# Kernel optimization log

Hardware: AMD Instinct MI355X
Metric: run time of the kernel (lower is better)

Reference implementation:

```python
import jax, jax.numpy as jnp
import numpy as np

N = 50000   # nodes
E = 800000  # edges
K = 3       # hops per TAGConv


def _row_normalize(x):
    row_sum = jnp.clip(jnp.sum(x, axis=1, keepdims=True), 1e-8, None)
    return x / row_sum


def _gcn_norm(edge_index, num_nodes):
    # PyG gcn_norm with add_self_loops=False (TAGConv default), edge_weight=1
    src, dst = edge_index[0], edge_index[1]
    deg = jax.ops.segment_sum(jnp.ones((src.shape[0],), jnp.float32), dst,
                              num_segments=num_nodes)
    deg_inv_sqrt = jnp.where(deg > 0, jnp.where(deg > 0, deg, 1.0) ** -0.5, 0.0)
    return deg_inv_sqrt[src] * deg_inv_sqrt[dst]  # [E]


def _propagate(x, src, dst, norm, num_nodes):
    # out[dst] += norm * x[src]   (sparse sym-normalized SpMM)
    return jax.ops.segment_sum(norm[:, None] * x[src], dst, num_segments=num_nodes)


def _tagconv(x, edge_index, norm, W, b):
    # W: [K+1, d_in, d_out]; out = sum_k A_hat^k x @ W_k + b
    src, dst = edge_index[0], edge_index[1]
    n = x.shape[0]
    hops = [x]
    for _ in range(W.shape[0] - 1):
        hops.append(_propagate(hops[-1], src, dst, norm, n))
    H = jnp.stack(hops)  # [K+1, N, d_in]
    return jnp.einsum('knd,kdo->no', H, W) + b


def setup_inputs() -> dict:
    key = jax.random.key(0)
    k1, k2, k3, k4 = jax.random.split(key, 4)
    x = jax.random.normal(k1, (N, 128), jnp.float32)
    edge_index = jax.random.randint(k2, (2, E), 0, N, jnp.int32)
    W1 = jax.random.normal(k3, (K + 1, 128, 16), jnp.float32) * 0.1
    b1 = jnp.zeros((16,), jnp.float32)
    W2 = jax.random.normal(k4, (K + 1, 16, 64), jnp.float32) * 0.1
    b2 = jnp.zeros((64,), jnp.float32)
    return {"x": x, "edge_index": edge_index, "W1": W1, "b1": b1,
            "W2": W2, "b2": b2}


def reference(x, edge_index, W1, b1, W2, b2):
    n = x.shape[0]
    norm = _gcn_norm(edge_index, n)
    h = _row_normalize(x)
    h = jax.nn.relu(_tagconv(h, edge_index, norm, W1, b1))
    # dropout is identity in eval mode
    return _tagconv(h, edge_index, norm, W2, b2)
```

## Files before the change

kernel.cpp:

```cpp
#include <hip/hip_runtime.h>
#include <hip/hip_bf16.h>

typedef unsigned short u16;

__device__ __forceinline__ float bf2f(u16 h) {
    return __uint_as_float(((unsigned int)h) << 16);
}
__device__ __forceinline__ u16 f2bf(float f) {
    __hip_bfloat16 h = __float2bfloat16(f);
    return *reinterpret_cast<u16*>(&h);
}

#define BKT_SHIFT 7
#define BKT_SIZE  128
#define CHUNK     2048

__global__ __launch_bounds__(256) void hist_kernel(const int* __restrict__ dst,
                                                   int* __restrict__ hist,
                                                   int E, int nbA, int nbuck) {
    __shared__ int lh[512];
    for (int j = threadIdx.x; j < nbuck; j += 256) lh[j] = 0;
    __syncthreads();
    int base = blockIdx.x * CHUNK;
    int end  = min(E, base + CHUNK);
    for (int e = base + threadIdx.x; e < end; e += 256)
        atomicAdd(&lh[dst[e] >> BKT_SHIFT], 1);
    __syncthreads();
    for (int j = threadIdx.x; j < nbuck; j += 256)
        hist[j * nbA + blockIdx.x] = lh[j];
}

__global__ __launch_bounds__(256) void scanA_kernel(const int* __restrict__ in,
                                                    int* __restrict__ outp1,
                                                    int* __restrict__ bsum, int n) {
    __shared__ int lds[256];
    int i = blockIdx.x * 256 + threadIdx.x;
    int v = (i < n) ? in[i] : 0;
    lds[threadIdx.x] = v;
    __syncthreads();
    #pragma unroll
    for (int off = 1; off < 256; off <<= 1) {
        int t = (threadIdx.x >= off) ? lds[threadIdx.x - off] : 0;
        __syncthreads();
        lds[threadIdx.x] += t;
        __syncthreads();
    }
    if (i < n) outp1[i + 1] = lds[threadIdx.x];
    if (threadIdx.x == 255) bsum[blockIdx.x] = lds[255];
}
__global__ __launch_bounds__(1024) void scanB_kernel(int* __restrict__ bsum, int nb) {
    __shared__ int lds[1024];
    int t = threadIdx.x;
    int v = (t < nb) ? bsum[t] : 0;
    lds[t] = v;
    __syncthreads();
    #pragma unroll
    for (int off = 1; off < 1024; off <<= 1) {
        int u = (t >= off) ? lds[t - off] : 0;
        __syncthreads();
        lds[t] += u;
        __syncthreads();
    }
    if (t < nb) bsum[t] = lds[t] - v;
}
__global__ __launch_bounds__(256) void scanC_kernel(int* __restrict__ outp1,
                                                    const int* __restrict__ bsum, int n) {
    int i = blockIdx.x * 256 + threadIdx.x;
    if (i < n) outp1[i + 1] += bsum[blockIdx.x];
    if (i == 0) outp1[0] = 0;
}

__global__ __launch_bounds__(256) void bucket_scatter_kernel(
    const int* __restrict__ src, const int* __restrict__ dst,
    const int* __restrict__ hofs, int2* __restrict__ bucketed,
    int E, int nbA, int nbuck)
{
    __shared__ int lbase[512];
    __shared__ int lcnt[512];
    for (int j = threadIdx.x; j < nbuck; j += 256) {
        lbase[j] = hofs[j * nbA + blockIdx.x];
        lcnt[j] = 0;
    }
    __syncthreads();
    int base = blockIdx.x * CHUNK;
    int end  = min(E, base + CHUNK);
    for (int e = base + threadIdx.x; e < end; e += 256) {
        int d = dst[e];
        int b = d >> BKT_SHIFT;
        int r = atomicAdd(&lcnt[b], 1);
        bucketed[lbase[b] + r] = make_int2(src[e], d);
    }
}

__global__ __launch_bounds__(256) void csr_finalize_kernel(
    const int2* __restrict__ bucketed, const int* __restrict__ hofs,
    int* __restrict__ rowptr, float* __restrict__ dis,
    float2* __restrict__ ecolw, int E, int nbA, int nbuck, int n)
{
    __shared__ int cnt[BKT_SIZE];
    __shared__ int run[BKT_SIZE];
    __shared__ float disl[BKT_SIZE];
    int b = blockIdx.x;
    int bstart = hofs[b * nbA];
    int bend   = (b == nbuck - 1) ? E : hofs[(b + 1) * nbA];
    for (int j = threadIdx.x; j < BKT_SIZE; j += 256) cnt[j] = 0;
    __syncthreads();
    for (int i = bstart + threadIdx.x; i < bend; i += 256)
        atomicAdd(&cnt[bucketed[i].y & (BKT_SIZE - 1)], 1);
    __syncthreads();
    if (threadIdx.x == 0) {
        int runacc = 0;
        for (int j = 0; j < BKT_SIZE; ++j) {
            int c = cnt[j];
            run[j] = runacc;
            runacc += c;
        }
    }
    __syncthreads();
    for (int j = threadIdx.x; j < BKT_SIZE; j += 256) {
        int d = b * BKT_SIZE + j;
        if (d < n) {
            rowptr[d] = bstart + run[j];
            int c = cnt[j];
            float dv = (c > 0) ? rsqrtf((float)c) : 0.0f;
            dis[d] = dv;
            disl[j] = dv;
        }
    }
    if (b == 0 && threadIdx.x == 0) rowptr[n] = E;
    __syncthreads();
    for (int i = bstart + threadIdx.x; i < bend; i += 256) {
        int2 p = bucketed[i];
        int j = p.y & (BKT_SIZE - 1);
        int r = atomicAdd(&run[j], 1);
        ecolw[bstart + r] = make_float2(__int_as_float(p.x), disl[j]);
    }
}

__global__ __launch_bounds__(256) void weight_kernel(float2* __restrict__ ecolw,
                                                     const float* __restrict__ dis, int E) {
    int e = blockIdx.x * blockDim.x + threadIdx.x;
    if (e < E) {
        float2 c = ecolw[e];
        ecolw[e].y = c.y * dis[__float_as_int(c.x)];
    }
}

__global__ __launch_bounds__(256) void gemm1_bf_kernel(
    const float* __restrict__ x, const float* __restrict__ W1,
    u16* __restrict__ zb, int n, int nstride)
{
    __shared__ float As[64 * 132];
    __shared__ float Bs[64 * 64];
    __shared__ float sums[128];
    const int t  = threadIdx.x;
    const int tx = t & 15;
    const int ty = t >> 4;
    const int c  = t & 15;
    const int g  = t >> 4;
    const int block_row = blockIdx.x * 128;

    float acc[8][4];
    #pragma unroll
    for (int i = 0; i < 8; ++i)
        #pragma unroll
        for (int j = 0; j < 4; ++j) acc[i][j] = 0.f;

    for (int kp = 0; kp < 2; ++kp) {
        #pragma unroll
        for (int i = 0; i < 8; ++i) {
            int row  = g + 16 * i;
            int grow = block_row + row;
            float v0 = 0.f, v1 = 0.f, v2 = 0.f, v3 = 0.f;
            if (grow < n) {
                const float* xp = x + (long)grow * 128 + kp * 64 + c;
                v0 = xp[0]; v1 = xp[16]; v2 = xp[32]; v3 = xp[48];
            }
            As[(c +  0) * 132 + row] = v0;
            As[(c + 16) * 132 + row] = v1;
            As[(c + 32) * 132 + row] = v2;
            As[(c + 48) * 132 + row] = v3;
            float red = (v0 + v1) + (v2 + v3);
            #pragma unroll
            for (int off = 8; off > 0; off >>= 1) red += __shfl_down(red, off, 16);
            if (c == 0) { if (kp == 0) sums[row] = red; else sums[row] += red; }
        }
        #pragma unroll
        for (int i2 = 0; i2 < 4; ++i2) {
            int kk = g + 16 * i2;
            int kglob = kp * 64 + kk;
            float4 wv = *(const float4*)(W1 + (c >> 2) * 2048 + kglob * 16 + 4 * (c & 3));
            *(float4*)(Bs + kk * 64 + 4 * c) = wv;
        }
        __syncthreads();
        #pragma unroll 4
        for (int kk = 0; kk < 64; ++kk) {
            float4 a0 = *(const float4*)(As + kk * 132 + 8 * ty);
            float4 a1 = *(const float4*)(As + kk * 132 + 8 * ty + 4);
            float4 bv = *(const float4*)(Bs + kk * 64 + 4 * tx);
            float ar[8] = {a0.x, a0.y, a0.z, a0.w, a1.x, a1.y, a1.z, a1.w};
            float br[4] = {bv.x, bv.y, bv.z, bv.w};
            #pragma unroll
            for (int i = 0; i < 8; ++i)
                #pragma unroll
                for (int j = 0; j < 4; ++j)
                    acc[i][j] += ar[i] * br[j];
        }
        __syncthreads();
    }
    int plane = tx >> 2;
    int oo4   = 4 * (tx & 3);
    #pragma unroll
    for (int i = 0; i < 8; ++i) {
        int row  = 8 * ty + i;
        int grow = block_row + row;
        if (grow < n) {
            float s = 1.0f / fmaxf(sums[row], 1e-8f);
            ushort4 o;
            o.x = f2bf(acc[i][0] * s); o.y = f2bf(acc[i][1] * s);
            o.z = f2bf(acc[i][2] * s); o.w = f2bf(acc[i][3] * s);
            *(ushort4*)(zb + (long)plane * nstride + (long)grow * 16 + oo4) = o;
        }
    }
}

__global__ __launch_bounds__(256) void spmm_csr_bf_kernel(
    const u16* __restrict__ in, const u16* __restrict__ addsrc,
    u16* __restrict__ out, const int* __restrict__ rowptr,
    const float2* __restrict__ ecolw, const float* __restrict__ b,
    int relu, int n)
{
    int t = blockIdx.x * blockDim.x + threadIdx.x;
    int r = t >> 3, q = t & 7;
    if (r >= n) return;
    int e0 = rowptr[r], e1 = rowptr[r + 1];
    float ax0=0,ay0=0, ax1=0,ay1=0, ax2=0,ay2=0, ax3=0,ay3=0;
    int e = e0;
    for (; e + 4 <= e1; e += 4) {
        float2 c0 = ecolw[e], c1 = ecolw[e+1], c2 = ecolw[e+2], c3 = ecolw[e+3];
        ushort2 v0 = *((const ushort2*)(in + (size_t)__float_as_int(c0.x) * 16) + q);
        ushort2 v1 = *((const ushort2*)(in + (size_t)__float_as_int(c1.x) * 16) + q);
        ushort2 v2 = *((const ushort2*)(in + (size_t)__float_as_int(c2.x) * 16) + q);
        ushort2 v3 = *((const ushort2*)(in + (size_t)__float_as_int(c3.x) * 16) + q);
        ax0 += c0.y * bf2f(v0.x); ay0 += c0.y * bf2f(v0.y);
        ax1 += c1.y * bf2f(v1.x); ay1 += c1.y * bf2f(v1.y);
        ax2 += c2.y * bf2f(v2.x); ay2 += c2.y * bf2f(v2.y);
        ax3 += c3.y * bf2f(v3.x); ay3 += c3.y * bf2f(v3.y);
    }
    for (; e < e1; ++e) {
        float2 c0 = ecolw[e];
        ushort2 v0 = *((const ushort2*)(in + (size_t)__float_as_int(c0.x) * 16) + q);
        ax0 += c0.y * bf2f(v0.x); ay0 += c0.y * bf2f(v0.y);
    }
    float Ax = (ax0 + ax1) + (ax2 + ax3);
    float Ay = (ay0 + ay1) + (ay2 + ay3);
    if (addsrc) {
        ushort2 s = *((const ushort2*)(addsrc + (size_t)r * 16) + q);
        Ax += bf2f(s.x); Ay += bf2f(s.y);
    }
    if (b) {
        Ax += b[2 * q];
        Ay += b[2 * q + 1];
    }
    if (relu) {
        Ax = fmaxf(Ax, 0.f);
        Ay = fmaxf(Ay, 0.f);
    }
    ushort2 o; o.x = f2bf(Ax); o.y = f2bf(Ay);
    *((ushort2*)(out + (size_t)r * 16) + q) = o;
}

__global__ __launch_bounds__(256) void gemm2_bf_kernel(
    const u16* __restrict__ zb, const float* __restrict__ W2,
    const float* __restrict__ b2, float* __restrict__ out, int n, int nstride)
{
    __shared__ float As[64 * 132];
    __shared__ float Bs[64 * 64];
    const int t  = threadIdx.x;
    const int tx = t & 15;
    const int ty = t >> 4;
    const int c  = t & 15;
    const int g  = t >> 4;
    const int block_row = blockIdx.x * 128;

    float acc[8][4];
    #pragma unroll
    for (int i = 0; i < 8; ++i)
        #pragma unroll
        for (int j = 0; j < 4; ++j) acc[i][j] = 0.f;

    #pragma unroll
    for (int i = 0; i < 8; ++i) {
        int row  = g + 16 * i;
        int grow = block_row + row;
        float v0 = 0.f, v1 = 0.f, v2 = 0.f, v3 = 0.f;
        if (grow < n) {
            const u16* zp = zb + (long)grow * 16 + c;
            v0 = bf2f(zp[0]);
            v1 = bf2f(zp[(long)nstride]);
            v2 = bf2f(zp[2 * (long)nstride]);
            v3 = bf2f(zp[3 * (long)nstride]);
        }
        As[(c +  0) * 132 + row] = v0;
        As[(c + 16) * 132 + row] = v1;
        As[(c + 32) * 132 + row] = v2;
        As[(c + 48) * 132 + row] = v3;
    }
    #pragma unroll
    for (int i2 = 0; i2 < 4; ++i2) {
        int j = g + 16 * i2;
        float4 wv = *(const float4*)(W2 + j * 64 + 4 * c);
        *(float4*)(Bs + j * 64 + 4 * c) = wv;
    }
    __syncthreads();
    #pragma unroll 4
    for (int kk = 0; kk < 64; ++kk) {
        float4 a0 = *(const float4*)(As + kk * 132 + 8 * ty);
        float4 a1 = *(const float4*)(As + kk * 132 + 8 * ty + 4);
        float4 bv = *(const float4*)(Bs + kk * 64 + 4 * tx);
        float ar[8] = {a0.x, a0.y, a0.z, a0.w, a1.x, a1.y, a1.z, a1.w};
        float br[4] = {bv.x, bv.y, bv.z, bv.w};
        #pragma unroll
        for (int i = 0; i < 8; ++i)
            #pragma unroll
            for (int j = 0; j < 4; ++j)
                acc[i][j] += ar[i] * br[j];
    }
    float4 bias = *(const float4*)(b2 + 4 * tx);
    #pragma unroll
    for (int i = 0; i < 8; ++i) {
        int grow = block_row + 8 * ty + i;
        if (grow < n) {
            float4 o = make_float4(acc[i][0] + bias.x, acc[i][1] + bias.y,
                                   acc[i][2] + bias.z, acc[i][3] + bias.w);
            *(float4*)(out + (long)grow * 64 + 4 * tx) = o;
        }
    }
}

__global__ void deg_kernel(const int* __restrict__ dst, float* __restrict__ deg, int E) {
    int e = blockIdx.x * blockDim.x + threadIdx.x;
    if (e < E) atomicAdd(&deg[dst[e]], 1.0f);
}
__global__ void disf_kernel(float* __restrict__ deg, int n) {
    int i = blockIdx.x * blockDim.x + threadIdx.x;
    if (i < n) {
        float d = deg[i];
        deg[i] = (d > 0.0f) ? rsqrtf(d) : 0.0f;
    }
}
__global__ __launch_bounds__(256) void gemm1_f32_kernel(
    const float* __restrict__ x, const float* __restrict__ W1,
    float* __restrict__ z, int n, int nstride)
{
    __shared__ float As[64 * 132];
    __shared__ float Bs[64 * 64];
    __shared__ float sums[128];
    const int t  = threadIdx.x;
    const int tx = t & 15;
    const int ty = t >> 4;
    const int c  = t & 15;
    const int g  = t >> 4;
    const int block_row = blockIdx.x * 128;
    float acc[8][4];
    #pragma unroll
    for (int i = 0; i < 8; ++i)
        #pragma unroll
        for (int j = 0; j < 4; ++j) acc[i][j] = 0.f;
    for (int kp = 0; kp < 2; ++kp) {
        #pragma unroll
        for (int i = 0; i < 8; ++i) {
            int row  = g + 16 * i;
            int grow = block_row + row;
            float v0 = 0.f, v1 = 0.f, v2 = 0.f, v3 = 0.f;
            if (grow < n) {
                const float* xp = x + (long)grow * 128 + kp * 64 + c;
                v0 = xp[0]; v1 = xp[16]; v2 = xp[32]; v3 = xp[48];
            }
            As[(c +  0) * 132 + row] = v0;
            As[(c + 16) * 132 + row] = v1;
            As[(c + 32) * 132 + row] = v2;
            As[(c + 48) * 132 + row] = v3;
            float red = (v0 + v1) + (v2 + v3);
            #pragma unroll
            for (int off = 8; off > 0; off >>= 1) red += __shfl_down(red, off, 16);
            if (c == 0) { if (kp == 0) sums[row] = red; else sums[row] += red; }
        }
        #pragma unroll
        for (int i2 = 0; i2 < 4; ++i2) {
            int kk = g + 16 * i2;
            int kglob = kp * 64 + kk;
            float4 wv = *(const float4*)(W1 + (c >> 2) * 2048 + kglob * 16 + 4 * (c & 3));
            *(float4*)(Bs + kk * 64 + 4 * c) = wv;
        }
        __syncthreads();
        #pragma unroll 4
        for (int kk = 0; kk < 64; ++kk) {
            float4 a0 = *(const float4*)(As + kk * 132 + 8 * ty);
            float4 a1 = *(const float4*)(As + kk * 132 + 8 * ty + 4);
            float4 bv = *(const float4*)(Bs + kk * 64 + 4 * tx);
            float ar[8] = {a0.x, a0.y, a0.z, a0.w, a1.x, a1.y, a1.z, a1.w};
            float br[4] = {bv.x, bv.y, bv.z, bv.w};
            #pragma unroll
            for (int i = 0; i < 8; ++i)
                #pragma unroll
                for (int j = 0; j < 4; ++j)
                    acc[i][j] += ar[i] * br[j];
        }
        __syncthreads();
    }
    int plane = tx >> 2;
    int oo4   = 4 * (tx & 3);
    #pragma unroll
    for (int i = 0; i < 8; ++i) {
        int row  = 8 * ty + i;
        int grow = block_row + row;
        if (grow < n) {
            float s = 1.0f / fmaxf(sums[row], 1e-8f);
            float4 o = make_float4(acc[i][0] * s, acc[i][1] * s, acc[i][2] * s, acc[i][3] * s);
            *(float4*)(z + (long)plane * nstride + (long)grow * 16 + oo4) = o;
        }
    }
}
__global__ __launch_bounds__(256) void spmm_atomic_kernel(
    const float* __restrict__ in, float* __restrict__ out,
    const int* __restrict__ src, const int* __restrict__ dst,
    const float* __restrict__ dis, int E)
{
    int t = blockIdx.x * blockDim.x + threadIdx.x;
    int e = t >> 4, f = t & 15;
    if (e < E) {
        int s = src[e], d = dst[e];
        atomicAdd(&out[d * 16 + f], dis[s] * dis[d] * in[s * 16 + f]);
    }
}
__global__ void bias_relu_kernel(float* __restrict__ z0, const float* __restrict__ b, int total) {
    int i = blockIdx.x * blockDim.x + threadIdx.x;
    if (i < total) {
        float v = z0[i] + b[i & 15];
        z0[i] = v > 0.0f ? v : 0.0f;
    }
}
__global__ __launch_bounds__(256) void gemm2_f32_kernel(
    const float* __restrict__ z, const float* __restrict__ W2,
    const float* __restrict__ b2, float* __restrict__ out, int n, int nstride)
{
    __shared__ float As[64 * 132];
    __shared__ float Bs[64 * 64];
    const int t  = threadIdx.x;
    const int tx = t & 15;
    const int ty = t >> 4;
    const int c  = t & 15;
    const int g  = t >> 4;
    const int block_row = blockIdx.x * 128;
    float acc[8][4];
    #pragma unroll
    for (int i = 0; i < 8; ++i)
        #pragma unroll
        for (int j = 0; j < 4; ++j) acc[i][j] = 0.f;
    #pragma unroll
    for (int i = 0; i < 8; ++i) {
        int row  = g + 16 * i;
        int grow = block_row + row;
        float v0 = 0.f, v1 = 0.f, v2 = 0.f, v3 = 0.f;
        if (grow < n) {
            const float* zp = z + (long)grow * 16 + c;
            v0 = zp[0];
            v1 = zp[(long)nstride];
            v2 = zp[2 * (long)nstride];
            v3 = zp[3 * (long)nstride];
        }
        As[(c +  0) * 132 + row] = v0;
        As[(c + 16) * 132 + row] = v1;
        As[(c + 32) * 132 + row] = v2;
        As[(c + 48) * 132 + row] = v3;
    }
    #pragma unroll
    for (int i2 = 0; i2 < 4; ++i2) {
        int j = g + 16 * i2;
        float4 wv = *(const float4*)(W2 + j * 64 + 4 * c);
        *(float4*)(Bs + j * 64 + 4 * c) = wv;
    }
    __syncthreads();
    #pragma unroll 4
    for (int kk = 0; kk < 64; ++kk) {
        float4 a0 = *(const float4*)(As + kk * 132 + 8 * ty);
        float4 a1 = *(const float4*)(As + kk * 132 + 8 * ty + 4);
        float4 bv = *(const float4*)(Bs + kk * 64 + 4 * tx);
        float ar[8] = {a0.x, a0.y, a0.z, a0.w, a1.x, a1.y, a1.z, a1.w};
        float br[4] = {bv.x, bv.y, bv.z, bv.w};
        #pragma unroll
        for (int i = 0; i < 8; ++i)
            #pragma unroll
            for (int j = 0; j < 4; ++j)
                acc[i][j] += ar[i] * br[j];
    }
    float4 bias = *(const float4*)(b2 + 4 * tx);
    #pragma unroll
    for (int i = 0; i < 8; ++i) {
        int grow = block_row + 8 * ty + i;
        if (grow < n) {
            float4 o = make_float4(acc[i][0] + bias.x, acc[i][1] + bias.y,
                                   acc[i][2] + bias.z, acc[i][3] + bias.w);
            *(float4*)(out + (long)grow * 64 + 4 * tx) = o;
        }
    }
}

static inline size_t align16(size_t v) { return (v + 15) & ~(size_t)15; }

extern "C" void kernel_launch(void* const* d_in, const int* in_sizes, int n_in,
                              void* d_out, int out_size, void* d_ws, size_t ws_size,
                              hipStream_t stream) {
    const float* x   = (const float*)d_in[0];
    const int*   ei  = (const int*)d_in[1];
    const float* W1  = (const float*)d_in[2];
    const float* b1  = (const float*)d_in[3];
    const float* W2  = (const float*)d_in[4];
    const float* bb2 = (const float*)d_in[5];
    float* out = (float*)d_out;

    const int n  = in_sizes[0] / 128;
    const int E  = in_sizes[1] / 2;
    const int NS = n * 16;

    const int* srcp = ei;
    const int* dstp = ei + E;

    const int nbuck = (n + BKT_SIZE - 1) >> BKT_SHIFT;
    const int nbA   = (E + CHUNK - 1) / CHUNK;
    const int m     = nbuck * nbA;
    const int nbS   = (m + 255) / 256;

    char* wsb = (char*)d_ws;
    int*   hist   = (int*)wsb;
    int*   hofs   = (int*)(wsb + (size_t)4 * m);
    int*   bsum   = (int*)(wsb + (size_t)4 * (2 * m + 1));
    int*   rowptr = (int*)(wsb + (size_t)4 * (2 * m + 1 + 1024));
    float* dis    = (float*)(wsb + (size_t)4 * (2 * m + 1 + 1024 + n + 1));
    size_t zoffb  = align16((size_t)4 * (2 * m + 1 + 1024 + 2 * n + 1));
    u16*   zb     = (u16*)(wsb + zoffb);
    size_t bkoff  = align16(zoffb + (size_t)2 * 4 * NS);
    int2*  bucketed = (int2*)(wsb + bkoff);
    size_t ecooff = align16(bkoff + (size_t)8 * E);
    float2* ecolw = (float2*)(wsb + ecooff);
    size_t need   = ecooff + (size_t)8 * E;

    int gemm_blocks = (n + 127) / 128;

    if (ws_size >= need && nbuck <= 512 && nbS <= 1024) {
        hist_kernel<<<nbA, 256, 0, stream>>>(dstp, hist, E, nbA, nbuck);
        scanA_kernel<<<nbS, 256, 0, stream>>>(hist, hofs, bsum, m);
        scanB_kernel<<<1, 1024, 0, stream>>>(bsum, nbS);
        scanC_kernel<<<nbS, 256, 0, stream>>>(hofs, bsum, m);
        bucket_scatter_kernel<<<nbA, 256, 0, stream>>>(srcp, dstp, hofs, bucketed, E, nbA, nbuck);
        csr_finalize_kernel<<<nbuck, 256, 0, stream>>>(bucketed, hofs, rowptr, dis, ecolw, E, nbA, nbuck, n);
        weight_kernel<<<(E + 255) / 256, 256, 0, stream>>>(ecolw, dis, E);

        gemm1_bf_kernel<<<gemm_blocks, 256, 0, stream>>>(x, W1, zb, n, NS);

        int sb = (8 * n + 255) / 256;
        spmm_csr_bf_kernel<<<sb, 256, 0, stream>>>(zb + 3 * NS, zb + 2 * NS, zb + 2 * NS, rowptr, ecolw, nullptr, 0, n);
        spmm_csr_bf_kernel<<<sb, 256, 0, stream>>>(zb + 2 * NS, zb + 1 * NS, zb + 1 * NS, rowptr, ecolw, nullptr, 0, n);
        spmm_csr_bf_kernel<<<sb, 256, 0, stream>>>(zb + 1 * NS, zb,          zb,          rowptr, ecolw, b1,      1, n);
        spmm_csr_bf_kernel<<<sb, 256, 0, stream>>>(zb,          nullptr, zb + 1 * NS, rowptr, ecolw, nullptr, 0, n);
        spmm_csr_bf_kernel<<<sb, 256, 0, stream>>>(zb + 1 * NS, nullptr, zb + 2 * NS, rowptr, ecolw, nullptr, 0, n);
        spmm_csr_bf_kernel<<<sb, 256, 0, stream>>>(zb + 2 * NS, nullptr, zb + 3 * NS, rowptr, ecolw, nullptr, 0, n);

        gemm2_bf_kernel<<<gemm_blocks, 256, 0, stream>>>(zb, W2, bb2, out, n, NS);
    } else {
        float* ws = (float*)d_ws;
        float* dis2 = ws;
        size_t z2off = ((size_t)n + 3) & ~(size_t)3;
        float* z2 = ws + z2off;
        hipMemsetAsync(dis2, 0, n * sizeof(float), stream);
        deg_kernel<<<(E + 255) / 256, 256, 0, stream>>>(dstp, dis2, E);
        disf_kernel<<<(n + 255) / 256, 256, 0, stream>>>(dis2, n);
        gemm1_f32_kernel<<<gemm_blocks, 256, 0, stream>>>(x, W1, z2, n, NS);
        int sb = (16 * E + 255) / 256;
        spmm_atomic_kernel<<<sb, 256, 0, stream>>>(z2 + 3 * NS, z2 + 2 * NS, srcp, dstp, dis2, E);
        spmm_atomic_kernel<<<sb, 256, 0, stream>>>(z2 + 2 * NS, z2 + 1 * NS, srcp, dstp, dis2, E);
        spmm_atomic_kernel<<<sb, 256, 0, stream>>>(z2 + 1 * NS, z2,          srcp, dstp, dis2, E);
        bias_relu_kernel<<<(NS + 255) / 256, 256, 0, stream>>>(z2, b1, NS);
        hipMemsetAsync(z2 + NS, 0, (size_t)3 * NS * sizeof(float), stream);
        spmm_atomic_kernel<<<sb, 256, 0, stream>>>(z2,          z2 + NS,     srcp, dstp, dis2, E);
        spmm_atomic_kernel<<<sb, 256, 0, stream>>>(z2 + NS,     z2 + 2 * NS, srcp, dstp, dis2, E);
        spmm_atomic_kernel<<<sb, 256, 0, stream>>>(z2 + 2 * NS, z2 + 3 * NS, srcp, dstp, dis2, E);
        gemm2_f32_kernel<<<gemm_blocks, 256, 0, stream>>>(z2, W2, bb2, out, n, NS);
    }
}
```

Before: 215.3 us.

## Factor symmetric norm into per-node scales and drop per-edge weights

Replaces the per-edge weight array with index-only CSR columns by factoring D^-1/2 A D^-1/2 into per-node row and column scalings. Gemm1 pre-scales the propagated planes by dis, and the SpMM scales by dis (or dis squared) at the row end. The second layer writes extra pre-scaled temporaries, so the edge loop only gathers and sums. This halves edge-array traffic and removes the weight_kernel launch, at the cost of extra workspace and additional bf16 writes of the scaled copies.

```diff
diff --git a/kernel.cpp b/kernel.cpp
--- a/kernel.cpp
+++ b/kernel.cpp
@@ -2,9 +2,10 @@
 #include <hip/hip_bf16.h>
 
 typedef unsigned short u16;
+typedef unsigned int u32;
 
 __device__ __forceinline__ float bf2f(u16 h) {
-    return __uint_as_float(((unsigned int)h) << 16);
+    return __uint_as_float(((u32)h) << 16);
 }
 __device__ __forceinline__ u16 f2bf(float f) {
     __hip_bfloat16 h = __float2bfloat16(f);
@@ -95,11 +96,10 @@
 __global__ __launch_bounds__(256) void csr_finalize_kernel(
     const int2* __restrict__ bucketed, const int* __restrict__ hofs,
     int* __restrict__ rowptr, float* __restrict__ dis,
-    float2* __restrict__ ecolw, int E, int nbA, int nbuck, int n)
+    u32* __restrict__ ecol, int E, int nbA, int nbuck, int n)
 {
     __shared__ int cnt[BKT_SIZE];
     __shared__ int run[BKT_SIZE];
-    __shared__ float disl[BKT_SIZE];
     int b = blockIdx.x;
     int bstart = hofs[b * nbA];
     int bend   = (b == nbuck - 1) ? E : hofs[(b + 1) * nbA];
@@ -122,9 +122,7 @@
         if (d < n) {
             rowptr[d] = bstart + run[j];
             int c = cnt[j];
-            float dv = (c > 0) ? rsqrtf((float)c) : 0.0f;
-            dis[d] = dv;
-            disl[j] = dv;
+            dis[d] = (c > 0) ? rsqrtf((float)c) : 0.0f;
         }
     }
     if (b == 0 && threadIdx.x == 0) rowptr[n] = E;
@@ -133,22 +131,13 @@
         int2 p = bucketed[i];
         int j = p.y & (BKT_SIZE - 1);
         int r = atomicAdd(&run[j], 1);
-        ecolw[bstart + r] = make_float2(__int_as_float(p.x), disl[j]);
-    }
-}
-
-__global__ __launch_bounds__(256) void weight_kernel(float2* __restrict__ ecolw,
-                                                     const float* __restrict__ dis, int E) {
-    int e = blockIdx.x * blockDim.x + threadIdx.x;
-    if (e < E) {
-        float2 c = ecolw[e];
-        ecolw[e].y = c.y * dis[__float_as_int(c.x)];
+        ecol[bstart + r] = (u32)p.x;
     }
 }
 
 __global__ __launch_bounds__(256) void gemm1_bf_kernel(
     const float* __restrict__ x, const float* __restrict__ W1,
-    u16* __restrict__ zb, int n, int nstride)
+    const float* __restrict__ dis, u16* __restrict__ zb, int n, int nstride)
 {
     __shared__ float As[64 * 132];
     __shared__ float Bs[64 * 64];
@@ -216,6 +205,7 @@
         int grow = block_row + row;
         if (grow < n) {
             float s = 1.0f / fmaxf(sums[row], 1e-8f);
+            if (plane != 0) s *= dis[grow];
             ushort4 o;
             o.x = f2bf(acc[i][0] * s); o.y = f2bf(acc[i][1] * s);
             o.z = f2bf(acc[i][2] * s); o.w = f2bf(acc[i][3] * s);
@@ -226,9 +216,10 @@
 
 __global__ __launch_bounds__(256) void spmm_csr_bf_kernel(
     const u16* __restrict__ in, const u16* __restrict__ addsrc,
-    u16* __restrict__ out, const int* __restrict__ rowptr,
-    const float2* __restrict__ ecolw, const float* __restrict__ b,
-    int relu, int n)
+    u16* __restrict__ out1, u16* __restrict__ out2,
+    const int* __restrict__ rowptr, const u32* __restrict__ ecol,
+    const float* __restrict__ dis, const float* __restrict__ b,
+    int relu, int sq1, int n)
 {
     int t = blockIdx.x * blockDim.x + threadIdx.x;
     int r = t >> 3, q = t & 7;
@@ -237,23 +228,25 @@
     float ax0=0,ay0=0, ax1=0,ay1=0, ax2=0,ay2=0, ax3=0,ay3=0;
     int e = e0;
     for (; e + 4 <= e1; e += 4) {
-        float2 c0 = ecolw[e], c1 = ecolw[e+1], c2 = ecolw[e+2], c3 = ecolw[e+3];
-        ushort2 v0 = *((const ushort2*)(in + (size_t)__float_as_int(c0.x) * 16) + q);
-        ushort2 v1 = *((const ushort2*)(in + (size_t)__float_as_int(c1.x) * 16) + q);
-        ushort2 v2 = *((const ushort2*)(in + (size_t)__float_as_int(c2.x) * 16) + q);
-        ushort2 v3 = *((const ushort2*)(in + (size_t)__float_as_int(c3.x) * 16) + q);
-        ax0 += c0.y * bf2f(v0.x); ay0 += c0.y * bf2f(v0.y);
-        ax1 += c1.y * bf2f(v1.x); ay1 += c1.y * bf2f(v1.y);
-        ax2 += c2.y * bf2f(v2.x); ay2 += c2.y * bf2f(v2.y);
-        ax3 += c3.y * bf2f(v3.x); ay3 += c3.y * bf2f(v3.y);
+        u32 s0 = ecol[e], s1 = ecol[e+1], s2 = ecol[e+2], s3 = ecol[e+3];
+        ushort2 v0 = *((const ushort2*)(in + (size_t)s0 * 16) + q);
+        ushort2 v1 = *((const ushort2*)(in + (size_t)s1 * 16) + q);
+        ushort2 v2 = *((const ushort2*)(in + (size_t)s2 * 16) + q);
+        ushort2 v3 = *((const ushort2*)(in + (size_t)s3 * 16) + q);
+        ax0 += bf2f(v0.x); ay0 += bf2f(v0.y);
+        ax1 += bf2f(v1.x); ay1 += bf2f(v1.y);
+        ax2 += bf2f(v2.x); ay2 += bf2f(v2.y);
+        ax3 += bf2f(v3.x); ay3 += bf2f(v3.y);
     }
     for (; e < e1; ++e) {
-        float2 c0 = ecolw[e];
-        ushort2 v0 = *((const ushort2*)(in + (size_t)__float_as_int(c0.x) * 16) + q);
-        ax0 += c0.y * bf2f(v0.x); ay0 += c0.y * bf2f(v0.y);
-    }
-    float Ax = (ax0 + ax1) + (ax2 + ax3);
-    float Ay = (ay0 + ay1) + (ay2 + ay3);
+        ushort2 v0 = *((const ushort2*)(in + (size_t)ecol[e] * 16) + q);
+        ax0 += bf2f(v0.x); ay0 += bf2f(v0.y);
+    }
+    float Sx = (ax0 + ax1) + (ax2 + ax3);
+    float Sy = (ay0 + ay1) + (ay2 + ay3);
+    float d1 = dis[r];
+    float sc1 = sq1 ? d1 * d1 : d1;
+    float Ax = Sx * sc1, Ay = Sy * sc1;
     if (addsrc) {
         ushort2 s = *((const ushort2*)(addsrc + (size_t)r * 16) + q);
         Ax += bf2f(s.x); Ay += bf2f(s.y);
@@ -267,7 +260,11 @@
         Ay = fmaxf(Ay, 0.f);
     }
     ushort2 o; o.x = f2bf(Ax); o.y = f2bf(Ay);
-    *((ushort2*)(out + (size_t)r * 16) + q) = o;
+    *((ushort2*)(out1 + (size_t)r * 16) + q) = o;
+    if (out2) {
+        ushort2 o2; o2.x = f2bf(Ax * d1); o2.y = f2bf(Ay * d1);
+        *((ushort2*)(out2 + (size_t)r * 16) + q) = o2;
+    }
 }
 
 __global__ __launch_bounds__(256) void gemm2_bf_kernel(
@@ -540,13 +537,15 @@
     float* dis    = (float*)(wsb + (size_t)4 * (2 * m + 1 + 1024 + n + 1));
     size_t zoffb  = align16((size_t)4 * (2 * m + 1 + 1024 + 2 * n + 1));
     u16*   zb     = (u16*)(wsb + zoffb);
-    size_t bkoff  = align16(zoffb + (size_t)2 * 4 * NS);
+    size_t bkoff  = align16(zoffb + (size_t)2 * 6 * NS);
     int2*  bucketed = (int2*)(wsb + bkoff);
     size_t ecooff = align16(bkoff + (size_t)8 * E);
-    float2* ecolw = (float2*)(wsb + ecooff);
-    size_t need   = ecooff + (size_t)8 * E;
+    u32*   ecol   = (u32*)(wsb + ecooff);
+    size_t need   = ecooff + (size_t)4 * E;
 
     int gemm_blocks = (n + 127) / 128;
+    u16 *P0 = zb, *P1 = zb + NS, *P2 = zb + 2 * NS, *P3 = zb + 3 * NS;
+    u16 *T0 = zb + 4 * NS, *T1 = zb + 5 * NS;
 
     if (ws_size >= need && nbuck <= 512 && nbS <= 1024) {
         hist_kernel<<<nbA, 256, 0, stream>>>(dstp, hist, E, nbA, nbuck);
@@ -554,18 +553,17 @@
         scanB_kernel<<<1, 1024, 0, stream>>>(bsum, nbS);
         scanC_kernel<<<nbS, 256, 0, stream>>>(hofs, bsum, m);
         bucket_scatter_kernel<<<nbA, 256, 0, stream>>>(srcp, dstp, hofs, bucketed, E, nbA, nbuck);
-        csr_finalize_kernel<<<nbuck, 256, 0, stream>>>(bucketed, hofs, rowptr, dis, ecolw, E, nbA, nbuck, n);
-        weight_kernel<<<(E + 255) / 256, 256, 0, stream>>>(ecolw, dis, E);
-
-        gemm1_bf_kernel<<<gemm_blocks, 256, 0, stream>>>(x, W1, zb, n, NS);
+        csr_finalize_kernel<<<nbuck, 256, 0, stream>>>(bucketed, hofs, rowptr, dis, ecol, E, nbA, nbuck, n);
+
+        gemm1_bf_kernel<<<gemm_blocks, 256, 0, stream>>>(x, W1, dis, zb, n, NS);
 
         int sb = (8 * n + 255) / 256;
-        spmm_csr_bf_kernel<<<sb, 256, 0, stream>>>(zb + 3 * NS, zb + 2 * NS, zb + 2 * NS, rowptr, ecolw, nullptr, 0, n);
-        spmm_csr_bf_kernel<<<sb, 256, 0, stream>>>(zb + 2 * NS, zb + 1 * NS, zb + 1 * NS, rowptr, ecolw, nullptr, 0, n);
-        spmm_csr_bf_kernel<<<sb, 256, 0, stream>>>(zb + 1 * NS, zb,          zb,          rowptr, ecolw, b1,      1, n);
-        spmm_csr_bf_kernel<<<sb, 256, 0, stream>>>(zb,          nullptr, zb + 1 * NS, rowptr, ecolw, nullptr, 0, n);
-        spmm_csr_bf_kernel<<<sb, 256, 0, stream>>>(zb + 1 * NS, nullptr, zb + 2 * NS, rowptr, ecolw, nullptr, 0, n);
-        spmm_csr_bf_kernel<<<sb, 256, 0, stream>>>(zb + 2 * NS, nullptr, zb + 3 * NS, rowptr, ecolw, nullptr, 0, n);
+        spmm_csr_bf_kernel<<<sb, 256, 0, stream>>>(P3, P2, P2, nullptr, rowptr, ecol, dis, nullptr, 0, 1, n);
+        spmm_csr_bf_kernel<<<sb, 256, 0, stream>>>(P2, P1, P1, nullptr, rowptr, ecol, dis, nullptr, 0, 1, n);
+        spmm_csr_bf_kernel<<<sb, 256, 0, stream>>>(P1, P0, P0, T0, rowptr, ecol, dis, b1, 1, 0, n);
+        spmm_csr_bf_kernel<<<sb, 256, 0, stream>>>(T0, nullptr, P1, T1, rowptr, ecol, dis, nullptr, 0, 0, n);
+        spmm_csr_bf_kernel<<<sb, 256, 0, stream>>>(T1, nullptr, P2, T0, rowptr, ecol, dis, nullptr, 0, 0, n);
+        spmm_csr_bf_kernel<<<sb, 256, 0, stream>>>(T0, nullptr, P3, nullptr, rowptr, ecol, dis, nullptr, 0, 0, n);
 
         gemm2_bf_kernel<<<gemm_blocks, 256, 0, stream>>>(zb, W2, bb2, out, n, NS);
     } else {
```

After: 206.2 us. 1.04x faster.
